# Optimization experiments

Measured on AMD Instinct MI355X. Metric: run time of the kernel, lower is better.

The kernel has to match this reference:

```python
import jax, jax.numpy as jnp
import numpy as np

GRID_SIZE = 5
SPLINE_ORDER = 3
B = 524288


def make_grid(in_features, grid_size=GRID_SIZE, spline_order=SPLINE_ORDER, grid_range=(-1.0, 1.0)):
    h = (grid_range[1] - grid_range[0]) / grid_size
    g = jnp.arange(-spline_order, grid_size + spline_order + 1, dtype=jnp.float32) * h + grid_range[0]
    return jnp.tile(g[None, :], (in_features, 1))  # (in, grid_size + 2*order + 1)


def b_splines(x, grid, order=SPLINE_ORDER):
    # x: (B, in), grid: (in, G). Cox-de Boor recursion, matching efficient-kan.
    xe = x[:, :, None]  # (B, in, 1)
    g = grid[None, :, :]  # (1, in, G)
    bases = ((xe >= g[:, :, :-1]) & (xe < g[:, :, 1:])).astype(x.dtype)
    for k in range(1, order + 1):
        left = (xe - g[:, :, : -(k + 1)]) / (g[:, :, k:-1] - g[:, :, : -(k + 1)])
        right = (g[:, :, k + 1:] - xe) / (g[:, :, k + 1:] - g[:, :, 1:-k])
        bases = left * bases[:, :, :-1] + right * bases[:, :, 1:]
    return bases  # (B, in, grid_size + order)


def kan_linear(x, base_w, spline_w, scaler, grid):
    # base path: SiLU activation then dense
    base_out = jax.nn.silu(x) @ base_w.T  # (B, out)
    # spline path
    bs = b_splines(x, grid)  # (B, in, K)
    scaled_sw = spline_w * scaler[:, :, None]  # (out, in, K)
    spline_out = jnp.einsum('bik,oik->bo', bs, scaled_sw)
    return base_out + spline_out


def setup_inputs() -> dict:
    key = jax.random.key(0)
    ks = jax.random.split(key, 7)
    return {
        'x': jax.random.normal(ks[0], (B, 1), dtype=jnp.float32),
        'base_w1': jax.random.normal(ks[1], (8, 1), dtype=jnp.float32) * 0.5,
        'spline_w1': jax.random.normal(ks[2], (8, 1, GRID_SIZE + SPLINE_ORDER), dtype=jnp.float32) * 0.1,
        'scaler1': jax.random.normal(ks[3], (8, 1), dtype=jnp.float32) * 0.5,
        'base_w2': jax.random.normal(ks[4], (1, 8), dtype=jnp.float32) * 0.5,
        'spline_w2': jax.random.normal(ks[5], (1, 8, GRID_SIZE + SPLINE_ORDER), dtype=jnp.float32) * 0.1,
        'scaler2': jax.random.normal(ks[6], (1, 8), dtype=jnp.float32) * 0.5,
    }


def reference(x, base_w1, spline_w1, scaler1, base_w2, spline_w2, scaler2):
    grid1 = make_grid(1)
    grid2 = make_grid(8)
    h = kan_linear(x, base_w1, spline_w1, scaler1, grid1)  # (B, 8)
    out = kan_linear(h, base_w2, spline_w2, scaler2, grid2)  # (B, 1)
    return out
```

## Files before the change

kernel.cpp:

```cpp
#include <hip/hip_runtime.h>


#define NKNOT 12
#define NB 8
#define NINT 2048
#define XLO  (-9.0f)
#define XHI  (9.0f)
#define HSTEP ((XHI - XLO) / (float)NINT)
#define INVH ((float)NINT / (XHI - XLO))


__device__ __forceinline__ void bspline8(float t, float b[NB]) {
    float g[NKNOT];
#pragma unroll
    for (int j = 0; j < NKNOT; ++j) g[j] = (float)(j - 3) * 0.4f - 1.0f;

    float cur[NKNOT - 1];
#pragma unroll
    for (int j = 0; j < NKNOT - 1; ++j)
        cur[j] = (t >= g[j] && t < g[j + 1]) ? 1.0f : 0.0f;

#pragma unroll
    for (int k = 1; k <= 3; ++k) {
#pragma unroll
        for (int j = 0; j < NKNOT - 1 - k; ++j) {
            const float invl = 1.0f / (g[j + k] - g[j]);
            const float invr = 1.0f / (g[j + k + 1] - g[j + 1]);
            cur[j] = (t - g[j]) * invl * cur[j] +
                     (g[j + k + 1] - t) * invr * cur[j + 1];
        }
    }
#pragma unroll
    for (int j = 0; j < NB; ++j) b[j] = cur[j];
}

__device__ __forceinline__ float silu_f(float x) {
    return x / (1.0f + __expf(-x));
}

__device__ float kan2_eval(float xv,
                           const float* __restrict__ bw1,
                           const float* __restrict__ sw1,
                           const float* __restrict__ sc1,
                           const float* __restrict__ bw2,
                           const float* __restrict__ sw2,
                           const float* __restrict__ sc2) {
    float bs[NB];
    bspline8(xv, bs);
    float sx = silu_f(xv);

    float h[8];
#pragma unroll
    for (int o = 0; o < 8; ++o) {
        float acc = sx * bw1[o];
        float sc = sc1[o];
#pragma unroll
        for (int k = 0; k < NB; ++k)
            acc += bs[k] * (sw1[o * NB + k] * sc);
        h[o] = acc;
    }

    float acc = 0.0f;
#pragma unroll
    for (int o = 0; o < 8; ++o) {
        float hv = h[o];
        acc += silu_f(hv) * bw2[o];
        float bs2[NB];
        bspline8(hv, bs2);
        float sc = sc2[o];
#pragma unroll
        for (int k = 0; k < NB; ++k)
            acc += bs2[k] * (sw2[o * NB + k] * sc);
    }
    return acc;
}


__global__ __launch_bounds__(256) void kan2_build_lut(
    const float* __restrict__ bw1, const float* __restrict__ sw1,
    const float* __restrict__ sc1, const float* __restrict__ bw2,
    const float* __restrict__ sw2, const float* __restrict__ sc2,
    float4* __restrict__ lut)
{
    int tid = blockIdx.x * blockDim.x + threadIdx.x;
    int j = tid >> 2;
    int n = tid & 3;
    float t = XLO + ((float)j + (float)n * (1.0f / 3.0f)) * HSTEP;

    float y = kan2_eval(t, bw1, sw1, sc1, bw2, sw2, sc2);

    int lane = threadIdx.x & 63;
    int base = lane & ~3;
    float y0 = __shfl(y, base + 0);
    float y1 = __shfl(y, base + 1);
    float y2 = __shfl(y, base + 2);
    float y3 = __shfl(y, base + 3);

    if (n == 0) {
        float4 c;
        c.x = y0;
        c.y = 0.5f * (-11.0f * y0 + 18.0f * y1 - 9.0f * y2 + 2.0f * y3);
        c.z = 0.5f * ( 18.0f * y0 - 45.0f * y1 + 36.0f * y2 - 9.0f * y3);
        c.w = 0.5f * ( -9.0f * y0 + 27.0f * y1 - 27.0f * y2 + 9.0f * y3);
        lut[j] = c;
    }
}


__global__ __launch_bounds__(256) void kan2_apply(
    const float4* __restrict__ x4,
    const float4* __restrict__ lut,
    float4* __restrict__ out4, int n4)
{
    __shared__ float4 slut[NINT];
    int t = threadIdx.x;
#pragma unroll
    for (int k = 0; k < NINT / 256; ++k)
        slut[t + k * 256] = lut[t + k * 256];
    __syncthreads();

    int i = blockIdx.x * 256 + t;
    if (i >= n4) return;

    float4 xv = x4[i];
    float4 r;
    float v[4] = {xv.x, xv.y, xv.z, xv.w};
    float o[4];
#pragma unroll
    for (int c = 0; c < 4; ++c) {
        float s = (v[c] - XLO) * INVH;
        s = fminf(fmaxf(s, 0.0f), (float)NINT - 0.5f);
        int j = (int)s;
        float u = s - (float)j;
        float4 cf = slut[j];
        o[c] = ((cf.w * u + cf.z) * u + cf.y) * u + cf.x;
    }
    r.x = o[0]; r.y = o[1]; r.z = o[2]; r.w = o[3];
    out4[i] = r;
}

extern "C" void kernel_launch(void* const* d_in, const int* in_sizes, int n_in,
                              void* d_out, int out_size, void* d_ws, size_t ws_size,
                              hipStream_t stream) {
    const float* x   = (const float*)d_in[0];
    const float* bw1 = (const float*)d_in[1];
    const float* sw1 = (const float*)d_in[2];
    const float* sc1 = (const float*)d_in[3];
    const float* bw2 = (const float*)d_in[4];
    const float* sw2 = (const float*)d_in[5];
    const float* sc2 = (const float*)d_in[6];
    float* out = (float*)d_out;
    float4* lut = (float4*)d_ws;

    int n = in_sizes[0];
    int n4 = n / 4;

    kan2_build_lut<<<(NINT * 4) / 256, 256, 0, stream>>>(
        bw1, sw1, sc1, bw2, sw2, sc2, lut);

    kan2_apply<<<(n4 + 255) / 256, 256, 0, stream>>>(
        (const float4*)x, (const float4*)lut, (float4*)out, n4);
}
```

Before: 73.60 us.

## Fuse LUT build and apply into one persistent kernel with flag sync

Merges the LUT-building kernel and the apply kernel into a single launch of 256 persistent blocks. The first 32 blocks build the cubic LUT and publish completion through release/acquire flags in the workspace. All blocks prefetch their x values, spin on those flags, copy the LUT into shared memory, then evaluate with a grid-stride loop. This removes one kernel launch and the gap between the two kernels. The flags are never reset, so on later calls the consumers can read a LUT that is being rewritten, and the spin-wait relies on all blocks being resident at once.

```diff
diff --git a/kernel.cpp b/kernel.cpp
--- a/kernel.cpp
+++ b/kernel.cpp
@@ -8,6 +8,11 @@
 #define XHI  (9.0f)
 #define HSTEP ((XHI - XLO) / (float)NINT)
 #define INVH ((float)NINT / (XHI - XLO))
+
+#define NBLK 256
+#define BUILD_BLOCKS 32
+#define MAGIC1 0x1357ACE5u
+#define MAGIC2 0x2468BD1Fu
 
 
 __device__ __forceinline__ void bspline8(float t, float b[NB]) {
@@ -38,7 +43,7 @@
     return x / (1.0f + __expf(-x));
 }
 
-__device__ float kan2_eval(float xv,
+__device__ __forceinline__ float kan2_eval(float xv,
                            const float* __restrict__ bw1,
                            const float* __restrict__ sw1,
                            const float* __restrict__ sc1,
@@ -75,55 +80,7 @@
     return acc;
 }
 
-
-__global__ __launch_bounds__(256) void kan2_build_lut(
-    const float* __restrict__ bw1, const float* __restrict__ sw1,
-    const float* __restrict__ sc1, const float* __restrict__ bw2,
-    const float* __restrict__ sw2, const float* __restrict__ sc2,
-    float4* __restrict__ lut)
-{
-    int tid = blockIdx.x * blockDim.x + threadIdx.x;
-    int j = tid >> 2;
-    int n = tid & 3;
-    float t = XLO + ((float)j + (float)n * (1.0f / 3.0f)) * HSTEP;
-
-    float y = kan2_eval(t, bw1, sw1, sc1, bw2, sw2, sc2);
-
-    int lane = threadIdx.x & 63;
-    int base = lane & ~3;
-    float y0 = __shfl(y, base + 0);
-    float y1 = __shfl(y, base + 1);
-    float y2 = __shfl(y, base + 2);
-    float y3 = __shfl(y, base + 3);
-
-    if (n == 0) {
-        float4 c;
-        c.x = y0;
-        c.y = 0.5f * (-11.0f * y0 + 18.0f * y1 - 9.0f * y2 + 2.0f * y3);
-        c.z = 0.5f * ( 18.0f * y0 - 45.0f * y1 + 36.0f * y2 - 9.0f * y3);
-        c.w = 0.5f * ( -9.0f * y0 + 27.0f * y1 - 27.0f * y2 + 9.0f * y3);
-        lut[j] = c;
-    }
-}
-
-
-__global__ __launch_bounds__(256) void kan2_apply(
-    const float4* __restrict__ x4,
-    const float4* __restrict__ lut,
-    float4* __restrict__ out4, int n4)
-{
-    __shared__ float4 slut[NINT];
-    int t = threadIdx.x;
-#pragma unroll
-    for (int k = 0; k < NINT / 256; ++k)
-        slut[t + k * 256] = lut[t + k * 256];
-    __syncthreads();
-
-    int i = blockIdx.x * 256 + t;
-    if (i >= n4) return;
-
-    float4 xv = x4[i];
-    float4 r;
+__device__ __forceinline__ float4 horner4(const float4* slut, float4 xv) {
     float v[4] = {xv.x, xv.y, xv.z, xv.w};
     float o[4];
 #pragma unroll
@@ -135,8 +92,83 @@
         float4 cf = slut[j];
         o[c] = ((cf.w * u + cf.z) * u + cf.y) * u + cf.x;
     }
-    r.x = o[0]; r.y = o[1]; r.z = o[2]; r.w = o[3];
-    out4[i] = r;
+    float4 r; r.x = o[0]; r.y = o[1]; r.z = o[2]; r.w = o[3];
+    return r;
+}
+
+
+__global__ __launch_bounds__(256) void kan2_fused(
+    const float* __restrict__ bw1, const float* __restrict__ sw1,
+    const float* __restrict__ sc1, const float* __restrict__ bw2,
+    const float* __restrict__ sw2, const float* __restrict__ sc2,
+    float4* __restrict__ lut, unsigned int* __restrict__ flags,
+    const float4* __restrict__ x4, float4* __restrict__ out4, int n4)
+{
+    __shared__ float4 slut[NINT];
+    const int t   = threadIdx.x;
+    const int bid = blockIdx.x;
+    const int gid = bid * 256 + t;
+
+    if (bid < BUILD_BLOCKS) {
+        int j = gid >> 2;
+        int n = gid & 3;
+        float tt = XLO + ((float)j + (float)n * (1.0f / 3.0f)) * HSTEP;
+
+        float y = kan2_eval(tt, bw1, sw1, sc1, bw2, sw2, sc2);
+
+        int lane = t & 63;
+        int base = lane & ~3;
+        float y0 = __shfl(y, base + 0);
+        float y1 = __shfl(y, base + 1);
+        float y2 = __shfl(y, base + 2);
+        float y3 = __shfl(y, base + 3);
+
+        if (n == 0) {
+            float4 c;
+            c.x = y0;
+            c.y = 0.5f * (-11.0f * y0 + 18.0f * y1 - 9.0f * y2 + 2.0f * y3);
+            c.z = 0.5f * ( 18.0f * y0 - 45.0f * y1 + 36.0f * y2 - 9.0f * y3);
+            c.w = 0.5f * ( -9.0f * y0 + 27.0f * y1 - 27.0f * y2 + 9.0f * y3);
+            lut[j] = c;
+        }
+        __syncthreads();
+        if (t == 0) {
+            __hip_atomic_store(&flags[2 * bid + 1], MAGIC2,
+                               __ATOMIC_RELEASE, __HIP_MEMORY_SCOPE_AGENT);
+            __hip_atomic_store(&flags[2 * bid + 0], MAGIC1,
+                               __ATOMIC_RELEASE, __HIP_MEMORY_SCOPE_AGENT);
+        }
+    }
+
+    const int stride = NBLK * 256;
+    int i0 = gid;
+    int i1 = gid + stride;
+    bool va = i0 < n4, vb = i1 < n4;
+    float4 xa, xb;
+    if (va) xa = x4[i0];
+    if (vb) xb = x4[i1];
+
+    if (t == 0) {
+        for (int b = 0; b < BUILD_BLOCKS; ++b) {
+            while (__hip_atomic_load(&flags[2 * b + 0], __ATOMIC_ACQUIRE,
+                                     __HIP_MEMORY_SCOPE_AGENT) != MAGIC1)
+                __builtin_amdgcn_s_sleep(1);
+            while (__hip_atomic_load(&flags[2 * b + 1], __ATOMIC_ACQUIRE,
+                                     __HIP_MEMORY_SCOPE_AGENT) != MAGIC2)
+                __builtin_amdgcn_s_sleep(1);
+        }
+    }
+    __syncthreads();
+
+#pragma unroll
+    for (int k = 0; k < NINT / 256; ++k)
+        slut[t + k * 256] = lut[t + k * 256];
+    __syncthreads();
+
+    if (va) out4[i0] = horner4(slut, xa);
+    if (vb) out4[i1] = horner4(slut, xb);
+    for (int i = gid + 2 * stride; i < n4; i += stride)
+        out4[i] = horner4(slut, x4[i]);
 }
 
 extern "C" void kernel_launch(void* const* d_in, const int* in_sizes, int n_in,
@@ -150,14 +182,15 @@
     const float* sw2 = (const float*)d_in[5];
     const float* sc2 = (const float*)d_in[6];
     float* out = (float*)d_out;
+
     float4* lut = (float4*)d_ws;
+    unsigned int* flags =
+        (unsigned int*)((char*)d_ws + NINT * sizeof(float4));
 
     int n = in_sizes[0];
     int n4 = n / 4;
 
-    kan2_build_lut<<<(NINT * 4) / 256, 256, 0, stream>>>(
-        bw1, sw1, sc1, bw2, sw2, sc2, lut);
-
-    kan2_apply<<<(n4 + 255) / 256, 256, 0, stream>>>(
-        (const float4*)x, (const float4*)lut, (float4*)out, n4);
+    kan2_fused<<<NBLK, 256, 0, stream>>>(
+        bw1, sw1, sc1, bw2, sw2, sc2, lut, flags,
+        (const float4*)x, (float4*)out, n4);
 }
```

New measurement: 201.4 us. 2.74x slower.
